# Performance work log

Hardware: AMD Instinct MI355X
Metric: run time of the kernel (lower is better)

The kernel has to match this reference:

```python
import jax, jax.numpy as jnp
import numpy as np

VIS_DIM = 4096
HIDDEN_D = 4096
EMB_DIM = 512
B = 128
N_NEG = 2048


def setup_inputs() -> dict:
    key = jax.random.key(0)
    k = jax.random.split(key, 7)
    vfs = jax.random.normal(k[0], (B, VIS_DIM), dtype=jnp.float32)
    p_lfs = jax.random.normal(k[1], (B, EMB_DIM), dtype=jnp.float32)
    n_lfs = jax.random.normal(k[2], (N_NEG, EMB_DIM), dtype=jnp.float32)
    # Linear params (PyTorch layout: W [out, in], y = x @ W.T + b)
    s_h = 1.0 / np.sqrt(VIS_DIM)
    s_e = 1.0 / np.sqrt(HIDDEN_D)
    W_h = jax.random.uniform(k[3], (HIDDEN_D, VIS_DIM), jnp.float32, -s_h, s_h)
    b_h = jax.random.uniform(k[4], (HIDDEN_D,), jnp.float32, -s_h, s_h)
    W_e = jax.random.uniform(k[5], (EMB_DIM, HIDDEN_D), jnp.float32, -s_e, s_e)
    b_e = jax.random.uniform(k[6], (EMB_DIM,), jnp.float32, -s_e, s_e)
    return {"vfs": vfs, "p_lfs": p_lfs, "n_lfs": n_lfs,
            "W_h": W_h, "b_h": b_h, "W_e": W_e, "b_e": b_e}


def _partial_order_sim(hypers, hypos):
    # -||relu(hypers - hypos)||_2 reduced over the last axis
    act = jax.nn.relu(hypers - hypos)
    return -jnp.sqrt(jnp.sum(act * act, axis=-1))


def reference(vfs, p_lfs, n_lfs, W_h, b_h, W_e, b_e):
    # Two plain Linears (NO ReLU in between, matching the original forward)
    vf_hidden = vfs @ W_h.T + b_h            # [B, 4096]
    vf_emb = vf_hidden @ W_e.T + b_e          # [B, emb]
    # positive score per sample
    p_scores = _partial_order_sim(p_lfs, vf_emb)                    # [B]
    # negative scores, batched over all samples at once (replaces per-sample loop)
    n_scores = _partial_order_sim(n_lfs[None, :, :], vf_emb[:, None, :])  # [B, N]
    score_stack = jnp.concatenate([p_scores[:, None], n_scores], axis=1)  # [B, N+1]
    return score_stack
```

## Files before the change

### kernel.cpp

```cpp
#include <hip/hip_runtime.h>

#define B_N  128
#define VIS  4096
#define HID  4096
#define EMB  512
#define NNEG 2048
#define OUTN (NNEG + 1)

using f32x4  = __attribute__((ext_vector_type(4))) float;
using bf16x8 = __attribute__((ext_vector_type(8))) short;

static __device__ __forceinline__ unsigned short f2bf(float f) {
  unsigned u = __builtin_bit_cast(unsigned, f);
  u += 0x7fffu + ((u >> 16) & 1u);
  return (unsigned short)(u >> 16);
}

union U16x8 { unsigned short us[8]; uint4 v; };
union U16x4 { unsigned short us[4]; uint2 v; };

static __device__ __forceinline__ void glds16(const void* g, void* l) {
  __builtin_amdgcn_global_load_lds(
      (const __attribute__((address_space(1))) unsigned*)g,
      (__attribute__((address_space(3))) unsigned*)l, 16, 0, 0);
}

__global__ __launch_bounds__(256) void prep_kernel(
    const float* __restrict__ src, unsigned short* __restrict__ dst) {
  const int idx = blockIdx.x * 256 + threadIdx.x;
  float4 a = ((const float4*)src)[idx * 2];
  float4 b = ((const float4*)src)[idx * 2 + 1];
  U16x8 pk;
  pk.us[0] = f2bf(a.x); pk.us[1] = f2bf(a.y); pk.us[2] = f2bf(a.z); pk.us[3] = f2bf(a.w);
  pk.us[4] = f2bf(b.x); pk.us[5] = f2bf(b.y); pk.us[6] = f2bf(b.z); pk.us[7] = f2bf(b.w);
  ((uint4*)dst)[idx] = pk.v;
}

__global__ __launch_bounds__(256, 2) void gemm1_kernel(
    const unsigned short* __restrict__ Abf, const float* __restrict__ Wh,
    const float* __restrict__ bh, float* __restrict__ Hf) {
  const int n0    = blockIdx.x * 32;
  const int kbase = blockIdx.y * 1024;

  __shared__ __align__(16) unsigned short As[128 * 64];
  __shared__ __align__(16) unsigned short Ws[32 * 64];

  const int t = threadIdx.x, w = t >> 6, lane = t & 63;
  const int m_lane = lane & 15, kq = lane >> 4;
  f32x4 acc[2][2] = {};

  const int wr = t >> 3, wc = (t & 7) * 8, Gw = t & 7;
  const float* Wg = Wh + (size_t)(n0 + wr) * VIS + kbase + wc;
  float4 wv0 = ((const float4*)Wg)[0];
  float4 wv1 = ((const float4*)Wg)[1];
  Wg += 64;

  const int rowA = lane >> 3;
  const int gA   = (lane & 7) ^ rowA;

  for (int kt = 0; kt < 16; ++kt) {
    __syncthreads();
#pragma unroll
    for (int i = 0; i < 4; ++i) {
      const int m = i * 32 + w * 8 + rowA;
      const unsigned short* src = Abf + (size_t)m * VIS + kbase + kt * 64 + gA * 8;
      glds16(src, &As[(i * 256 + w * 64) * 8]);
    }
    {
      U16x8 pk;
      pk.us[0] = f2bf(wv0.x); pk.us[1] = f2bf(wv0.y); pk.us[2] = f2bf(wv0.z); pk.us[3] = f2bf(wv0.w);
      pk.us[4] = f2bf(wv1.x); pk.us[5] = f2bf(wv1.y); pk.us[6] = f2bf(wv1.z); pk.us[7] = f2bf(wv1.w);
      *(uint4*)&Ws[wr * 64 + ((Gw ^ (wr & 7)) * 8)] = pk.v;
    }
    if (kt < 15) {
      wv0 = ((const float4*)Wg)[0];
      wv1 = ((const float4*)Wg)[1];
      Wg += 64;
    }
    __syncthreads();

#pragma unroll
    for (int ks = 0; ks < 2; ++ks) {
      const int Gk = ks * 4 + kq;
      const int m0 = w * 32 + m_lane, m1 = m0 + 16;
      bf16x8 a0 = *(const bf16x8*)&As[m0 * 64 + ((Gk ^ (m0 & 7)) * 8)];
      bf16x8 a1 = *(const bf16x8*)&As[m1 * 64 + ((Gk ^ (m1 & 7)) * 8)];
      const int nA = m_lane, nB = m_lane + 16;
      bf16x8 b0 = *(const bf16x8*)&Ws[nA * 64 + ((Gk ^ (nA & 7)) * 8)];
      bf16x8 b1 = *(const bf16x8*)&Ws[nB * 64 + ((Gk ^ (nB & 7)) * 8)];
      acc[0][0] = __builtin_amdgcn_mfma_f32_16x16x32_bf16(a0, b0, acc[0][0], 0, 0, 0);
      acc[0][1] = __builtin_amdgcn_mfma_f32_16x16x32_bf16(a0, b1, acc[0][1], 0, 0, 0);
      acc[1][0] = __builtin_amdgcn_mfma_f32_16x16x32_bf16(a1, b0, acc[1][0], 0, 0, 0);
      acc[1][1] = __builtin_amdgcn_mfma_f32_16x16x32_bf16(a1, b1, acc[1][1], 0, 0, 0);
    }
  }

  const int rq = (lane >> 4) * 4;
#pragma unroll
  for (int mi = 0; mi < 2; ++mi) {
#pragma unroll
    for (int ni = 0; ni < 2; ++ni) {
      const int ng = n0 + ni * 16 + m_lane;
      const float bias = (blockIdx.y == 0) ? bh[ng] : 0.0f;
#pragma unroll
      for (int r = 0; r < 4; ++r) {
        const int mg = w * 32 + mi * 16 + rq + r;
        atomicAdd(&Hf[(size_t)mg * HID + ng], acc[mi][ni][r] + bias);
      }
    }
  }
}

__global__ __launch_bounds__(256) void cvt_kernel(
    const float* __restrict__ src, unsigned short* __restrict__ dst) {
  const int idx = blockIdx.x * 256 + threadIdx.x;
  float4 a = ((const float4*)src)[idx * 2];
  float4 b = ((const float4*)src)[idx * 2 + 1];
  U16x8 pk;
  pk.us[0] = f2bf(a.x); pk.us[1] = f2bf(a.y); pk.us[2] = f2bf(a.z); pk.us[3] = f2bf(a.w);
  pk.us[4] = f2bf(b.x); pk.us[5] = f2bf(b.y); pk.us[6] = f2bf(b.z); pk.us[7] = f2bf(b.w);
  ((uint4*)dst)[idx] = pk.v;
}

__global__ __launch_bounds__(256, 2) void gemm2_kernel(
    const unsigned short* __restrict__ Hbf, const float* __restrict__ We,
    const float* __restrict__ be, float* __restrict__ emb) {
  const int n0    = blockIdx.x * 16;
  const int kbase = blockIdx.y * 512;

  __shared__ __align__(16) unsigned short As[128 * 64];
  __shared__ __align__(16) unsigned short Ws[16 * 64];

  const int t = threadIdx.x, w = t >> 6, lane = t & 63;
  const int m_lane = lane & 15, kq = lane >> 4;
  f32x4 acc[2] = {};

  const int wr = t >> 4, wc = (t & 15) * 4;
  const float* Wg = We + (size_t)(n0 + wr) * HID + kbase + wc;
  float4 wv = ((const float4*)Wg)[0];
  Wg += 64;

  const int rowA = lane >> 3;
  const int gA   = (lane & 7) ^ rowA;

  for (int kt = 0; kt < 8; ++kt) {
    __syncthreads();
#pragma unroll
    for (int i = 0; i < 4; ++i) {
      const int m = i * 32 + w * 8 + rowA;
      const unsigned short* src = Hbf + (size_t)m * HID + kbase + kt * 64 + gA * 8;
      glds16(src, &As[(i * 256 + w * 64) * 8]);
    }
    {
      U16x4 pk;
      pk.us[0] = f2bf(wv.x); pk.us[1] = f2bf(wv.y); pk.us[2] = f2bf(wv.z); pk.us[3] = f2bf(wv.w);
      const int G = (t & 15) >> 1;
      *(uint2*)&Ws[wr * 64 + ((G ^ (wr & 7)) * 8) + (t & 1) * 4] = pk.v;
    }
    if (kt < 7) { wv = ((const float4*)Wg)[0]; Wg += 64; }
    __syncthreads();

#pragma unroll
    for (int ks = 0; ks < 2; ++ks) {
      const int Gk = ks * 4 + kq;
      const int m0 = w * 32 + m_lane, m1 = m0 + 16;
      bf16x8 a0 = *(const bf16x8*)&As[m0 * 64 + ((Gk ^ (m0 & 7)) * 8)];
      bf16x8 a1 = *(const bf16x8*)&As[m1 * 64 + ((Gk ^ (m1 & 7)) * 8)];
      bf16x8 b0 = *(const bf16x8*)&Ws[m_lane * 64 + ((Gk ^ (m_lane & 7)) * 8)];
      acc[0] = __builtin_amdgcn_mfma_f32_16x16x32_bf16(a0, b0, acc[0], 0, 0, 0);
      acc[1] = __builtin_amdgcn_mfma_f32_16x16x32_bf16(a1, b0, acc[1], 0, 0, 0);
    }
  }

  const int rq = (lane >> 4) * 4;
  const int ng = n0 + m_lane;
  const float bias = (blockIdx.y == 0) ? be[ng] : 0.0f;
#pragma unroll
  for (int mi = 0; mi < 2; ++mi) {
#pragma unroll
    for (int r = 0; r < 4; ++r) {
      const int mg = w * 32 + mi * 16 + rq + r;
      atomicAdd(&emb[mg * EMB + ng], acc[mi][r] + bias);
    }
  }
}

__global__ __launch_bounds__(256, 2) void score_kernel(
    const float* __restrict__ emb, const float* __restrict__ n_lfs,
    const float* __restrict__ p_lfs, float* __restrict__ out) {
  const int bx = blockIdx.x;
  const int t = threadIdx.x;
  const int s = t & 15, tb = t >> 4;

  if (bx < 1024) {
    const int nc = bx >> 3, bt = bx & 7;
    const int n0 = nc * 16, b0 = bt * 16;
    __shared__ __align__(16) float nl[16 * 576];
#pragma unroll
    for (int i = 0; i < 8; ++i) {
      const int f = t + i * 256;
      const int r = f >> 7, o4 = f & 127;
      float4 v = *(const float4*)(n_lfs + (size_t)(n0 + r) * EMB + o4 * 4);
      *(float4*)&nl[r * 576 + (o4 >> 3) * 36 + (o4 & 7) * 4] = v;
    }
    const float* eb = emb + (size_t)(b0 + tb) * EMB + s * 32;
    float4 ev[8];
#pragma unroll
    for (int i = 0; i < 8; ++i) ev[i] = *(const float4*)(eb + i * 4);
    __syncthreads();

    for (int j = 0; j < 16; ++j) {
      const float* nr = &nl[j * 576 + s * 36];
      float a0 = 0.f, a1 = 0.f, a2 = 0.f, a3 = 0.f;
#pragma unroll
      for (int i = 0; i < 8; ++i) {
        float4 nv = *(const float4*)(nr + i * 4);
        float d0 = fmaxf(nv.x - ev[i].x, 0.f);
        float d1 = fmaxf(nv.y - ev[i].y, 0.f);
        float d2 = fmaxf(nv.z - ev[i].z, 0.f);
        float d3 = fmaxf(nv.w - ev[i].w, 0.f);
        a0 = fmaf(d0, d0, a0); a1 = fmaf(d1, d1, a1);
        a2 = fmaf(d2, d2, a2); a3 = fmaf(d3, d3, a3);
      }
      float ss = (a0 + a1) + (a2 + a3);
      ss += __shfl_xor(ss, 1);
      ss += __shfl_xor(ss, 2);
      ss += __shfl_xor(ss, 4);
      ss += __shfl_xor(ss, 8);
      if (s == 0) out[(size_t)(b0 + tb) * OUTN + 1 + n0 + j] = -sqrtf(ss);
    }
  } else {
    const int b = (bx - 1024) * 16 + tb;
    const float* eb = emb + (size_t)b * EMB + s * 32;
    const float* pb = p_lfs + (size_t)b * EMB + s * 32;
    float a0 = 0.f, a1 = 0.f, a2 = 0.f, a3 = 0.f;
#pragma unroll
    for (int i = 0; i < 8; ++i) {
      float4 pv = *(const float4*)(pb + i * 4);
      float4 ev = *(const float4*)(eb + i * 4);
      float d0 = fmaxf(pv.x - ev.x, 0.f);
      float d1 = fmaxf(pv.y - ev.y, 0.f);
      float d2 = fmaxf(pv.z - ev.z, 0.f);
      float d3 = fmaxf(pv.w - ev.w, 0.f);
      a0 = fmaf(d0, d0, a0); a1 = fmaf(d1, d1, a1);
      a2 = fmaf(d2, d2, a2); a3 = fmaf(d3, d3, a3);
    }
    float ss = (a0 + a1) + (a2 + a3);
    ss += __shfl_xor(ss, 1);
    ss += __shfl_xor(ss, 2);
    ss += __shfl_xor(ss, 4);
    ss += __shfl_xor(ss, 8);
    if (s == 0) out[(size_t)b * OUTN] = -sqrtf(ss);
  }
}

extern "C" void kernel_launch(void* const* d_in, const int* in_sizes, int n_in,
                              void* d_out, int out_size, void* d_ws, size_t ws_size,
                              hipStream_t stream) {
  const float* vfs   = (const float*)d_in[0];
  const float* p_lfs = (const float*)d_in[1];
  const float* n_lfs = (const float*)d_in[2];
  const float* W_h   = (const float*)d_in[3];
  const float* b_h   = (const float*)d_in[4];
  const float* W_e   = (const float*)d_in[5];
  const float* b_e   = (const float*)d_in[6];
  float* out = (float*)d_out;

  char* ws = (char*)d_ws;
  float*          Hf  = (float*)ws;
  float*          emb = (float*)(ws + (2u << 20));
  unsigned short* Abf = (unsigned short*)(ws + (2u << 20) + (256u << 10));
  unsigned short* Hbf = (unsigned short*)(ws + (3u << 20) + (256u << 10));

  hipMemsetAsync(Hf, 0, (2u << 20) + (256u << 10), stream);
  prep_kernel<<<256, 256, 0, stream>>>(vfs, Abf);
  gemm1_kernel<<<dim3(HID / 32, 4), 256, 0, stream>>>(Abf, W_h, b_h, Hf);
  cvt_kernel<<<256, 256, 0, stream>>>(Hf, Hbf);
  gemm2_kernel<<<dim3(EMB / 16, 8), 256, 0, stream>>>(Hbf, W_e, b_e, emb);
  score_kernel<<<1032, 256, 0, stream>>>(emb, n_lfs, p_lfs, out);
}
```

Measured before the change: 160.5 us.

## Replace gemm1 atomic split-K with two-way partial buffers and drop memset

```diff
diff --git a/kernel.cpp b/kernel.cpp
--- a/kernel.cpp
+++ b/kernel.cpp
@@ -26,7 +26,8 @@
 }
 
 __global__ __launch_bounds__(256) void prep_kernel(
-    const float* __restrict__ src, unsigned short* __restrict__ dst) {
+    const float* __restrict__ src, unsigned short* __restrict__ dst,
+    float* __restrict__ emb) {
   const int idx = blockIdx.x * 256 + threadIdx.x;
   float4 a = ((const float4*)src)[idx * 2];
   float4 b = ((const float4*)src)[idx * 2 + 1];
@@ -34,47 +35,46 @@
   pk.us[0] = f2bf(a.x); pk.us[1] = f2bf(a.y); pk.us[2] = f2bf(a.z); pk.us[3] = f2bf(a.w);
   pk.us[4] = f2bf(b.x); pk.us[5] = f2bf(b.y); pk.us[6] = f2bf(b.z); pk.us[7] = f2bf(b.w);
   ((uint4*)dst)[idx] = pk.v;
-}
-
-__global__ __launch_bounds__(256, 2) void gemm1_kernel(
+  if (idx < (B_N * EMB / 4))
+    ((float4*)emb)[idx] = make_float4(0.f, 0.f, 0.f, 0.f);
+}
+
+__global__ __launch_bounds__(512, 2) void gemm1_kernel(
     const unsigned short* __restrict__ Abf, const float* __restrict__ Wh,
-    const float* __restrict__ bh, float* __restrict__ Hf) {
+    const float* __restrict__ bh, float* __restrict__ Hp) {
   const int n0    = blockIdx.x * 32;
-  const int kbase = blockIdx.y * 1024;
+  const int kbase = blockIdx.y * 2048;
 
   __shared__ __align__(16) unsigned short As[128 * 64];
   __shared__ __align__(16) unsigned short Ws[32 * 64];
 
   const int t = threadIdx.x, w = t >> 6, lane = t & 63;
   const int m_lane = lane & 15, kq = lane >> 4;
-  f32x4 acc[2][2] = {};
-
-  const int wr = t >> 3, wc = (t & 7) * 8, Gw = t & 7;
+  f32x4 acc[2] = {};
+
+  const int wr = t >> 4, wc = (t & 15) * 4, Gw = (t & 15) >> 1, sub = (t & 1) * 4;
   const float* Wg = Wh + (size_t)(n0 + wr) * VIS + kbase + wc;
-  float4 wv0 = ((const float4*)Wg)[0];
-  float4 wv1 = ((const float4*)Wg)[1];
+  float4 wv = ((const float4*)Wg)[0];
   Wg += 64;
 
   const int rowA = lane >> 3;
   const int gA   = (lane & 7) ^ rowA;
 
-  for (int kt = 0; kt < 16; ++kt) {
-    __syncthreads();
-#pragma unroll
-    for (int i = 0; i < 4; ++i) {
-      const int m = i * 32 + w * 8 + rowA;
+  for (int kt = 0; kt < 32; ++kt) {
+    __syncthreads();
+#pragma unroll
+    for (int i = 0; i < 2; ++i) {
+      const int m = i * 64 + w * 8 + rowA;
       const unsigned short* src = Abf + (size_t)m * VIS + kbase + kt * 64 + gA * 8;
-      glds16(src, &As[(i * 256 + w * 64) * 8]);
+      glds16(src, &As[(i * 512 + w * 64) * 8]);
     }
     {
-      U16x8 pk;
-      pk.us[0] = f2bf(wv0.x); pk.us[1] = f2bf(wv0.y); pk.us[2] = f2bf(wv0.z); pk.us[3] = f2bf(wv0.w);
-      pk.us[4] = f2bf(wv1.x); pk.us[5] = f2bf(wv1.y); pk.us[6] = f2bf(wv1.z); pk.us[7] = f2bf(wv1.w);
-      *(uint4*)&Ws[wr * 64 + ((Gw ^ (wr & 7)) * 8)] = pk.v;
-    }
-    if (kt < 15) {
-      wv0 = ((const float4*)Wg)[0];
-      wv1 = ((const float4*)Wg)[1];
+      U16x4 pk;
+      pk.us[0] = f2bf(wv.x); pk.us[1] = f2bf(wv.y); pk.us[2] = f2bf(wv.z); pk.us[3] = f2bf(wv.w);
+      *(uint2*)&Ws[wr * 64 + ((Gw ^ (wr & 7)) * 8) + sub] = pk.v;
+    }
+    if (kt < 31) {
+      wv = ((const float4*)Wg)[0];
       Wg += 64;
     }
     __syncthreads();
@@ -82,43 +82,43 @@
 #pragma unroll
     for (int ks = 0; ks < 2; ++ks) {
       const int Gk = ks * 4 + kq;
-      const int m0 = w * 32 + m_lane, m1 = m0 + 16;
+      const int m0 = w * 16 + m_lane;
       bf16x8 a0 = *(const bf16x8*)&As[m0 * 64 + ((Gk ^ (m0 & 7)) * 8)];
-      bf16x8 a1 = *(const bf16x8*)&As[m1 * 64 + ((Gk ^ (m1 & 7)) * 8)];
       const int nA = m_lane, nB = m_lane + 16;
       bf16x8 b0 = *(const bf16x8*)&Ws[nA * 64 + ((Gk ^ (nA & 7)) * 8)];
       bf16x8 b1 = *(const bf16x8*)&Ws[nB * 64 + ((Gk ^ (nB & 7)) * 8)];
-      acc[0][0] = __builtin_amdgcn_mfma_f32_16x16x32_bf16(a0, b0, acc[0][0], 0, 0, 0);
-      acc[0][1] = __builtin_amdgcn_mfma_f32_16x16x32_bf16(a0, b1, acc[0][1], 0, 0, 0);
-      acc[1][0] = __builtin_amdgcn_mfma_f32_16x16x32_bf16(a1, b0, acc[1][0], 0, 0, 0);
-      acc[1][1] = __builtin_amdgcn_mfma_f32_16x16x32_bf16(a1, b1, acc[1][1], 0, 0, 0);
-    }
-  }
-
+      acc[0] = __builtin_amdgcn_mfma_f32_16x16x32_bf16(a0, b0, acc[0], 0, 0, 0);
+      acc[1] = __builtin_amdgcn_mfma_f32_16x16x32_bf16(a0, b1, acc[1], 0, 0, 0);
+    }
+  }
+
+  float* Pd = Hp + (size_t)blockIdx.y * (B_N * HID);
   const int rq = (lane >> 4) * 4;
 #pragma unroll
-  for (int mi = 0; mi < 2; ++mi) {
-#pragma unroll
-    for (int ni = 0; ni < 2; ++ni) {
-      const int ng = n0 + ni * 16 + m_lane;
-      const float bias = (blockIdx.y == 0) ? bh[ng] : 0.0f;
-#pragma unroll
-      for (int r = 0; r < 4; ++r) {
-        const int mg = w * 32 + mi * 16 + rq + r;
-        atomicAdd(&Hf[(size_t)mg * HID + ng], acc[mi][ni][r] + bias);
-      }
-    }
-  }
-}
-
-__global__ __launch_bounds__(256) void cvt_kernel(
-    const float* __restrict__ src, unsigned short* __restrict__ dst) {
+  for (int ni = 0; ni < 2; ++ni) {
+    const int ng = n0 + ni * 16 + m_lane;
+    const float bias = (blockIdx.y == 0) ? bh[ng] : 0.0f;
+#pragma unroll
+    for (int r = 0; r < 4; ++r) {
+      const int mg = w * 16 + rq + r;
+      Pd[(size_t)mg * HID + ng] = acc[ni][r] + bias;
+    }
+  }
+}
+
+__global__ __launch_bounds__(256) void cvt2_kernel(
+    const float* __restrict__ Hp, unsigned short* __restrict__ dst) {
   const int idx = blockIdx.x * 256 + threadIdx.x;
-  float4 a = ((const float4*)src)[idx * 2];
-  float4 b = ((const float4*)src)[idx * 2 + 1];
+  const float* H1 = Hp + (size_t)B_N * HID;
+  float4 a0 = ((const float4*)Hp)[idx * 2];
+  float4 b0 = ((const float4*)Hp)[idx * 2 + 1];
+  float4 a1 = ((const float4*)H1)[idx * 2];
+  float4 b1 = ((const float4*)H1)[idx * 2 + 1];
   U16x8 pk;
-  pk.us[0] = f2bf(a.x); pk.us[1] = f2bf(a.y); pk.us[2] = f2bf(a.z); pk.us[3] = f2bf(a.w);
-  pk.us[4] = f2bf(b.x); pk.us[5] = f2bf(b.y); pk.us[6] = f2bf(b.z); pk.us[7] = f2bf(b.w);
+  pk.us[0] = f2bf(a0.x + a1.x); pk.us[1] = f2bf(a0.y + a1.y);
+  pk.us[2] = f2bf(a0.z + a1.z); pk.us[3] = f2bf(a0.w + a1.w);
+  pk.us[4] = f2bf(b0.x + b1.x); pk.us[5] = f2bf(b0.y + b1.y);
+  pk.us[6] = f2bf(b0.z + b1.z); pk.us[7] = f2bf(b0.w + b1.w);
   ((uint4*)dst)[idx] = pk.v;
 }
 
@@ -267,15 +267,14 @@
   float* out = (float*)d_out;
 
   char* ws = (char*)d_ws;
-  float*          Hf  = (float*)ws;
-  float*          emb = (float*)(ws + (2u << 20));
-  unsigned short* Abf = (unsigned short*)(ws + (2u << 20) + (256u << 10));
-  unsigned short* Hbf = (unsigned short*)(ws + (3u << 20) + (256u << 10));
-
-  hipMemsetAsync(Hf, 0, (2u << 20) + (256u << 10), stream);
-  prep_kernel<<<256, 256, 0, stream>>>(vfs, Abf);
-  gemm1_kernel<<<dim3(HID / 32, 4), 256, 0, stream>>>(Abf, W_h, b_h, Hf);
-  cvt_kernel<<<256, 256, 0, stream>>>(Hf, Hbf);
+  float*          Hp  = (float*)ws;
+  float*          emb = (float*)(ws + (4u << 20));
+  unsigned short* Abf = (unsigned short*)(ws + (4u << 20) + (256u << 10));
+  unsigned short* Hbf = (unsigned short*)(ws + (5u << 20) + (256u << 10));
+
+  prep_kernel<<<256, 256, 0, stream>>>(vfs, Abf, emb);
+  gemm1_kernel<<<dim3(HID / 32, 2), 512, 0, stream>>>(Abf, W_h, b_h, Hp);
+  cvt2_kernel<<<256, 256, 0, stream>>>(Hp, Hbf);
   gemm2_kernel<<<dim3(EMB / 16, 8), 256, 0, stream>>>(Hbf, W_e, b_e, emb);
   score_kernel<<<1032, 256, 0, stream>>>(emb, n_lfs, p_lfs, out);
 }
```

Measured after the change: 170.7 us. +6.3%, slower.
